# Kernel tuning notes

Measured on AMD Instinct MI355X. Metric: run time of the kernel, lower is better.

The kernel has to match this reference:

```python
import jax, jax.numpy as jnp
import numpy as np

N = 50000      # nodes
E = 800000     # edges
B = 512        # graphs in batch
DRNL = 64      # drnl_dim (feature_dim = 0)
H = 256        # hidden


def setup_inputs() -> dict:
    key = jax.random.key(0)
    ks = jax.random.split(key, 12)
    x = jax.random.normal(ks[0], (N, DRNL), jnp.float32)
    edge_index = jax.random.randint(ks[1], (2, E), 0, N)
    batch_vec = jnp.sort(jax.random.randint(ks[2], (N,), 0, B))
    u_idx = jax.random.randint(ks[3], (B,), 0, N)
    v_idx = jax.random.randint(ks[4], (B,), 0, N)

    def glorot(k, shp):
        scale = jnp.sqrt(2.0 / (shp[0] + shp[1]))
        return (jax.random.normal(k, shp, jnp.float32) * scale).astype(jnp.float32)

    W0 = glorot(ks[5], (DRNL, H)); b0 = jnp.zeros((H,), jnp.float32)
    W1 = glorot(ks[6], (H, H));    b1 = jnp.zeros((H,), jnp.float32)
    W2 = glorot(ks[7], (H, H));    b2 = jnp.zeros((H,), jnp.float32)
    Wm1 = glorot(ks[8], (3 * H, H)); bm1 = jnp.zeros((H,), jnp.float32)
    Wm2 = glorot(ks[9], (H, 1));     bm2 = jnp.zeros((1,), jnp.float32)
    return dict(x=x, edge_index=edge_index, batch_vec=batch_vec,
                u_idx=u_idx, v_idx=v_idx,
                W0=W0, b0=b0, W1=W1, b1=b1, W2=W2, b2=b2,
                Wm1=Wm1, bm1=bm1, Wm2=Wm2, bm2=bm2)


def _gcn_encode(x, src, dst, Ws, bs):
    # Standard GCN: h' = D^-1/2 (A + I) D^-1/2 h W + b, ReLU between layers.
    n = x.shape[0]
    loop = jnp.arange(n)
    src2 = jnp.concatenate([src, loop])  # add self-loops
    dst2 = jnp.concatenate([dst, loop])
    deg = jax.ops.segment_sum(jnp.ones_like(dst2, x.dtype), dst2, num_segments=n)
    dis = jax.lax.rsqrt(jnp.maximum(deg, 1.0))          # D^-1/2
    norm = dis[src2] * dis[dst2]                         # per-edge norm [E+N]

    h = x
    for i, (W, b) in enumerate(zip(Ws, bs)):
        msg = h[src2] * norm[:, None]                    # gather + scale
        agg = jax.ops.segment_sum(msg, dst2, num_segments=n)
        h = agg @ W + b
        if i < len(Ws) - 1:
            h = jax.nn.relu(h)
    return h


def reference(x, edge_index, batch_vec, u_idx, v_idx,
              W0, b0, W1, b1, W2, b2, Wm1, bm1, Wm2, bm2):
    src, dst = edge_index[0], edge_index[1]
    h = _gcn_encode(x, src, dst, (W0, W1, W2), (b0, b1, b2))   # [N, H]

    # global_mean_pool over batch_vec -> [B, H]
    cnt = jax.ops.segment_sum(jnp.ones((h.shape[0],), h.dtype), batch_vec,
                              num_segments=B)
    g = jax.ops.segment_sum(h, batch_vec, num_segments=B) / \
        jnp.maximum(cnt, 1.0)[:, None]

    # concat [g, h[u], h[v]] -> MLP -> [B] logits
    z = jnp.concatenate([g, h[u_idx], h[v_idx]], axis=1)       # [B, 3H]
    z = jax.nn.relu(z @ Wm1 + bm1)
    return (z @ Wm2 + bm2).squeeze(-1)
```

## Files before the change

### kernel.cpp

```cpp
#include <hip/hip_runtime.h>
#include <hip/hip_bf16.h>
#include <stdint.h>

#ifndef DRNL
#define DRNL 64
#define HDIM 256
#endif

#define CHUNK 4096
#define BCAP 3072

typedef __attribute__((ext_vector_type(4))) float f32x4;
typedef __attribute__((ext_vector_type(8))) _Float16 f16x8;

__device__ __forceinline__ void async16(void* lds, const void* g) {
    __builtin_amdgcn_global_load_lds(
        (const __attribute__((address_space(1))) void*)g,
        (__attribute__((address_space(3))) void*)(char*)lds, 16, 0, 0);
}

__device__ __forceinline__ int imin(int a, int b) { return a < b ? a : b; }

__global__ __launch_bounds__(256) void k_misc(
    const int* __restrict__ batch,
    const float* __restrict__ x,
    const float* __restrict__ W0, const float* __restrict__ W1,
    const float* __restrict__ W2,
    int* __restrict__ gstart,
    _Float16* __restrict__ x16,
    _Float16* __restrict__ W0t, _Float16* __restrict__ W1t,
    _Float16* __restrict__ W2t,
    int N, int B) {
    const int gsz = gridDim.x * 256;
    const int gid0 = blockIdx.x * 256 + threadIdx.x;

    for (int i = gid0; i < (DRNL + 2 * HDIM) * 256; i += gsz) {
        int b = i >> 8, c = i & 255;
        const float* W; _Float16* T; int k, K;
        if (b < DRNL)            { W = W0; T = W0t; k = b;              K = DRNL; }
        else if (b < DRNL + 256) { W = W1; T = W1t; k = b - DRNL;       K = HDIM; }
        else                     { W = W2; T = W2t; k = b - DRNL - 256; K = HDIM; }
        T[(size_t)c * K + k] = (_Float16)W[(size_t)k * 256 + c];
    }

    for (int i = gid0; i < N * DRNL; i += gsz) x16[i] = (_Float16)x[i];

    for (int i = gid0; i <= N; i += gsz) {
        if (i == 0) {
            int b0 = batch[0];
            for (int b = 0; b <= b0; ++b) gstart[b] = 0;
        } else if (i == N) {
            int bl = batch[N - 1];
            for (int b = bl + 1; b <= B; ++b) gstart[b] = N;
        } else {
            int bp = batch[i - 1], bc = batch[i];
            if (bc != bp)
                for (int b = bp + 1; b <= bc; ++b) gstart[b] = i;
        }
    }
}

__global__ __launch_bounds__(256) void k_hist(const int* __restrict__ dst,
                                              int* __restrict__ ghist,
                                              int E, int P, int SH, int NBUCK) {
    __shared__ int h[512];
    int tid = threadIdx.x, p = blockIdx.x;
    for (int i = tid; i < NBUCK; i += 256) h[i] = 0;
    __syncthreads();
    int e0 = p * CHUNK, e1 = imin(e0 + CHUNK, E);
    for (int e = e0 + tid; e < e1; e += 256)
        atomicAdd(&h[dst[e] >> SH], 1);
    __syncthreads();
    for (int b = tid; b < NBUCK; b += 256)
        ghist[(size_t)b * P + p] = h[b];
}

__global__ __launch_bounds__(256) void k_gbase(int* __restrict__ ghist,
                                               int* __restrict__ btot, int P) {
    __shared__ int s[256];
    int b = blockIdx.x, tid = threadIdx.x;
    int* row = ghist + (size_t)b * P;
    int carry = 0;
    for (int base = 0; base < P; base += 256) {
        int idx = base + tid;
        int v = (idx < P) ? row[idx] : 0;
        s[tid] = v;
        __syncthreads();
        for (int o = 1; o < 256; o <<= 1) {
            int t = (tid >= o) ? s[tid - o] : 0;
            __syncthreads();
            s[tid] += t;
            __syncthreads();
        }
        if (idx < P) row[idx] = carry + s[tid] - v;
        carry += s[255];
        __syncthreads();
    }
    if (tid == 0) btot[b] = carry;
}

__global__ __launch_bounds__(256) void k_btscan(const int* __restrict__ btot,
                                                int* __restrict__ bbase,
                                                int* __restrict__ rowptr,
                                                int NBUCK, int N, int E) {
    __shared__ int s[256];
    int tid = threadIdx.x;
    int carry = 0;
    for (int base = 0; base < NBUCK; base += 256) {
        int idx = base + tid;
        int v = (idx < NBUCK) ? btot[idx] : 0;
        s[tid] = v;
        __syncthreads();
        for (int o = 1; o < 256; o <<= 1) {
            int t = (tid >= o) ? s[tid - o] : 0;
            __syncthreads();
            s[tid] += t;
            __syncthreads();
        }
        if (idx < NBUCK) bbase[idx] = carry + s[tid] - v;
        carry += s[255];
        __syncthreads();
    }
    if (tid == 0) { bbase[NBUCK] = E; rowptr[N] = E; }
}

__global__ __launch_bounds__(256) void k_scatter(const int* __restrict__ src,
                                                 const int* __restrict__ dst,
                                                 const int* __restrict__ ghist,
                                                 const int* __restrict__ bbase,
                                                 int* __restrict__ tmp,
                                                 int E, int P, int SH, int NBUCK) {
    __shared__ int base[512];
    int p = blockIdx.x, tid = threadIdx.x;
    for (int b = tid; b < NBUCK; b += 256)
        base[b] = bbase[b] + ghist[(size_t)b * P + p];
    __syncthreads();
    int e0 = p * CHUNK, e1 = imin(e0 + CHUNK, E);
    int msk = (1 << SH) - 1;
    for (int e = e0 + tid; e < e1; e += 256) {
        int d = dst[e];
        int r = atomicAdd(&base[d >> SH], 1);
        tmp[r] = (src[e] << SH) | (d & msk);
    }
}

__global__ __launch_bounds__(256) void k_bsort(const int* __restrict__ tmp,
                                               const int* __restrict__ bbase,
                                               int* __restrict__ col,
                                               int* __restrict__ rowptr,
                                               float* __restrict__ dis,
                                               _Float16* __restrict__ x16,
                                               int SH, int N) {
    __shared__ int cnt[512];
    __shared__ int off[512];
    __shared__ int sscan[256];
    __shared__ int eL[BCAP];
    __shared__ unsigned short rnk[BCAP];
    __shared__ int sL[BCAP];
    int b = blockIdx.x, tid = threadIdx.x;
    int nodes = 1 << SH, node0 = b << SH, msk = nodes - 1;
    int lo = bbase[b], hi = bbase[b + 1], m = hi - lo;
    bool fast = (m <= BCAP);

    for (int i = tid; i < nodes; i += 256) cnt[i] = 0;
    __syncthreads();
    if (fast) {
        for (int i = tid; i < m; i += 256) {
            int v = tmp[lo + i];
            eL[i] = v;
            rnk[i] = (unsigned short)atomicAdd(&cnt[v & msk], 1);
        }
    } else {
        for (int i = tid; i < m; i += 256)
            atomicAdd(&cnt[tmp[lo + i] & msk], 1);
    }
    __syncthreads();
    int carry = 0;
    for (int base = 0; base < nodes; base += 256) {
        int idx = base + tid;
        int v = (idx < nodes) ? cnt[idx] : 0;
        sscan[tid] = v;
        __syncthreads();
        for (int o = 1; o < 256; o <<= 1) {
            int t = (tid >= o) ? sscan[tid - o] : 0;
            __syncthreads();
            sscan[tid] += t;
            __syncthreads();
        }
        if (idx < nodes) off[idx] = carry + sscan[tid] - v;
        carry += sscan[255];
        __syncthreads();
    }
    for (int i = tid; i < nodes; i += 256) {
        int node = node0 + i;
        if (node < N) {
            rowptr[node] = lo + off[i];
            dis[node]    = rsqrtf((float)cnt[i] + 1.f);
        }
    }
    int rlim = imin(nodes, N - node0);
    for (int u = tid; u < rlim * 8; u += 256) {
        int r = u >> 3, c = u & 7;
        float d = rsqrtf((float)cnt[r] + 1.f);
        f16x8* xv = (f16x8*)(x16 + (size_t)(node0 + r) * 64);
        f16x8 v = xv[c];
        f16x8 o;
#pragma unroll
        for (int k = 0; k < 8; ++k) o[k] = (_Float16)((float)v[k] * d);
        xv[c] = o;
    }
    __syncthreads();
    if (fast) {
        for (int i = tid; i < m; i += 256) {
            int v = eL[i];
            sL[off[v & msk] + rnk[i]] = v >> SH;
        }
        __syncthreads();
        for (int i = tid; i < m; i += 256) col[lo + i] = sL[i];
    } else {
        for (int i = tid; i < nodes; i += 256) cnt[i] = 0;
        __syncthreads();
        for (int i = tid; i < m; i += 256) {
            int v = tmp[lo + i];
            int d = v & msk;
            int r = atomicAdd(&cnt[d], 1);
            col[lo + off[d] + r] = v >> SH;
        }
    }
}

template <int FBLK>
__global__ __launch_bounds__(256) void k_agg(const _Float16* __restrict__ hs,
                                             const float* __restrict__ dis,
                                             const int* __restrict__ rowptr,
                                             const int* __restrict__ col,
                                             _Float16* __restrict__ A16, int N) {
    int node_wg, f;
    if constexpr (FBLK == 4) {
        int wg = blockIdx.x;
        int xcd = wg & 7;
        f = xcd >> 1;
        int half = xcd & 1;
        int NH = gridDim.x >> 3;
        node_wg = half * NH + (wg >> 3);
    } else {
        node_wg = blockIdx.x;
        f = 0;
    }
    int lane = threadIdx.x & 63;
    int wv = threadIdx.x >> 6;
    int oct = lane >> 3;
    int fl = lane & 7;
    int gw = node_wg * 32 + wv * 8 + oct;
    bool valid = gw < N;
    int gwc = valid ? gw : N - 1;
    const size_t boff = (size_t)f * ((size_t)N * 64);
    const f16x8* hv = (const f16x8*)(hs + boff);
    float acc[8];
#pragma unroll
    for (int k = 0; k < 8; ++k) acc[k] = 0.f;

    int e0 = rowptr[gwc];
    int e1 = valid ? rowptr[gwc + 1] : e0;
    int j = e0;
    while (__any(j < e1)) {
        bool a0 = j < e1, a1 = j + 1 < e1, a2 = j + 2 < e1, a3 = j + 3 < e1;
        int s0 = col[a0 ? j : 0];
        int s1 = col[a1 ? j + 1 : 0];
        int s2 = col[a2 ? j + 2 : 0];
        int s3 = col[a3 ? j + 3 : 0];
        float m0 = a0 ? 1.f : 0.f, m1 = a1 ? 1.f : 0.f;
        float m2 = a2 ? 1.f : 0.f, m3 = a3 ? 1.f : 0.f;
        f16x8 v0 = hv[(size_t)s0 * 8 + fl];
        f16x8 v1 = hv[(size_t)s1 * 8 + fl];
        f16x8 v2 = hv[(size_t)s2 * 8 + fl];
        f16x8 v3 = hv[(size_t)s3 * 8 + fl];
#pragma unroll
        for (int k = 0; k < 8; ++k) acc[k] += m0 * (float)v0[k];
#pragma unroll
        for (int k = 0; k < 8; ++k) acc[k] += m1 * (float)v1[k];
#pragma unroll
        for (int k = 0; k < 8; ++k) acc[k] += m2 * (float)v2[k];
#pragma unroll
        for (int k = 0; k < 8; ++k) acc[k] += m3 * (float)v3[k];
        j += 4;
    }

    float dn = dis[gwc];
    f16x8 hsv = hv[(size_t)gwc * 8 + fl];
    f16x8 o;
#pragma unroll
    for (int k = 0; k < 8; ++k)
        o[k] = (_Float16)((acc[k] + (float)hsv[k]) * dn);
    if (valid)
        __builtin_nontemporal_store(
            o, (f16x8*)(A16 + boff + (size_t)gw * 64 + fl * 8));
}

template <int K, int OUT_RELU, int SCALE>
__global__ __launch_bounds__(256, 2) void k_mgemm(const _Float16* __restrict__ A,
                                                  const _Float16* __restrict__ W,
                                                  const float* __restrict__ bias,
                                                  const float* __restrict__ dis,
                                                  _Float16* __restrict__ outh, int n) {
    __shared__ _Float16 sA[128 * 32];
    __shared__ _Float16 sW[256 * 32];

    const int tid = threadIdx.x;
    const int lane = tid & 63;
    const int w = tid >> 6;
    const int c15 = lane & 15;
    const int q = lane >> 4;
    const int row0 = blockIdx.x * 128;
    const size_t bstride = (size_t)n * 64;

    f32x4 acc[8][4];
#pragma unroll
    for (int i = 0; i < 8; ++i)
#pragma unroll
        for (int j = 0; j < 4; ++j) acc[i][j] = (f32x4)0.f;

    for (int kt = 0; kt < K; kt += 32) {
#pragma unroll
        for (int i = 0; i < 2; ++i) {
            int u = tid + (i << 8);
            int row = u >> 2;
            int qq = (u & 3) ^ ((row >> 1) & 3);
            int r = imin(row0 + row, n - 1);
            size_t goff = (size_t)(kt >> 6) * bstride + (size_t)r * 64 + (kt & 63) + qq * 8;
            async16(sA + u * 8, A + goff);
        }
#pragma unroll
        for (int i = 0; i < 4; ++i) {
            int u = tid + (i << 8);
            int c = u >> 2;
            int qq = (u & 3) ^ ((c >> 1) & 3);
            size_t goff = (size_t)c * K + kt + qq * 8;
            async16(sW + u * 8, W + goff);
        }
        __syncthreads();

        f16x8 wf[4];
#pragma unroll
        for (int ct = 0; ct < 4; ++ct) {
            int c = (w << 6) + (ct << 4) + c15;
            int u = (c << 2) + (q ^ ((c >> 1) & 3));
            wf[ct] = *(const f16x8*)(sW + u * 8);
        }
#pragma unroll
        for (int rt = 0; rt < 8; ++rt) {
            int r = (rt << 4) + c15;
            int u = (r << 2) + (q ^ ((r >> 1) & 3));
            f16x8 a = *(const f16x8*)(sA + u * 8);
#pragma unroll
            for (int ct = 0; ct < 4; ++ct)
                acc[rt][ct] = __builtin_amdgcn_mfma_f32_16x16x32_f16(a, wf[ct], acc[rt][ct], 0, 0, 0);
        }
        __syncthreads();
    }

#pragma unroll
    for (int ct = 0; ct < 4; ++ct) {
        int c = (w << 6) + (ct << 4) + c15;
        float bv = bias[c];
        _Float16* ob = outh + (size_t)(c >> 6) * bstride + (c & 63);
#pragma unroll
        for (int rt = 0; rt < 8; ++rt) {
#pragma unroll
            for (int r = 0; r < 4; ++r) {
                int row = row0 + (rt << 4) + (q << 2) + r;
                if (row < n) {
                    float v = acc[rt][ct][r] + bv;
                    if (OUT_RELU) v = fmaxf(v, 0.f);
                    if (SCALE) v *= dis[row];
                    ob[(size_t)row * 64] = (_Float16)v;
                }
            }
        }
    }
}

__global__ __launch_bounds__(256) void k_head(const _Float16* __restrict__ h,
                                              const int* __restrict__ gstart,
                                              const int* __restrict__ u,
                                              const int* __restrict__ v,
                                              const float* __restrict__ Wm1,
                                              const float* __restrict__ bm1,
                                              const float* __restrict__ Wm2,
                                              const float* __restrict__ bm2,
                                              float* __restrict__ out, int N) {
    int b = blockIdx.x;
    int t = threadIdx.x;
    __shared__ float z[3 * HDIM];
    __shared__ float red[4];
    const _Float16* hb = h + (size_t)(t >> 6) * ((size_t)N * 64) + (t & 63);
    int s = gstart[b], e = gstart[b + 1];
    float pa = 0.f;
    int i = s;
    for (; i + 3 < e; i += 4) {
        float a0 = (float)hb[(size_t)i * 64];
        float a1 = (float)hb[(size_t)(i + 1) * 64];
        float a2 = (float)hb[(size_t)(i + 2) * 64];
        float a3 = (float)hb[(size_t)(i + 3) * 64];
        pa += (a0 + a1) + (a2 + a3);
    }
    for (; i < e; ++i) pa += (float)hb[(size_t)i * 64];
    z[t]            = pa / fmaxf((float)(e - s), 1.f);
    z[HDIM + t]     = (float)hb[(size_t)u[b] * 64];
    z[2 * HDIM + t] = (float)hb[(size_t)v[b] * 64];
    __syncthreads();
    float acc[8];
#pragma unroll
    for (int k = 0; k < 8; ++k) acc[k] = 0.f;
    for (int k = 0; k < 3 * HDIM; k += 8) {
#pragma unroll
        for (int jj = 0; jj < 8; ++jj)
            acc[jj] = fmaf(z[k + jj], Wm1[(size_t)(k + jj) * HDIM + t], acc[jj]);
    }
    float sum = (((acc[0] + acc[1]) + (acc[2] + acc[3])) +
                 ((acc[4] + acc[5]) + (acc[6] + acc[7]))) + bm1[t];
    float hid = fmaxf(sum, 0.f);
    float p = hid * Wm2[t];
    for (int off = 32; off; off >>= 1) p += __shfl_down(p, off);
    if ((t & 63) == 0) red[t >> 6] = p;
    __syncthreads();
    if (t == 0) out[b] = red[0] + red[1] + red[2] + red[3] + bm2[0];
}

extern "C" void kernel_launch(void* const* d_in, const int* in_sizes, int n_in,
                              void* d_out, int out_size, void* d_ws, size_t ws_size,
                              hipStream_t stream) {
    const float* x    = (const float*)d_in[0];
    const int*   ei   = (const int*)d_in[1];
    const int*   batc = (const int*)d_in[2];
    const int*   uidx = (const int*)d_in[3];
    const int*   vidx = (const int*)d_in[4];
    const float* W0   = (const float*)d_in[5];
    const float* b0   = (const float*)d_in[6];
    const float* W1   = (const float*)d_in[7];
    const float* b1   = (const float*)d_in[8];
    const float* W2   = (const float*)d_in[9];
    const float* b2   = (const float*)d_in[10];
    const float* Wm1  = (const float*)d_in[11];
    const float* bm1  = (const float*)d_in[12];
    const float* Wm2  = (const float*)d_in[13];
    const float* bm2  = (const float*)d_in[14];
    float* out = (float*)d_out;

    const int N = in_sizes[0] / DRNL;
    const int E = in_sizes[1] / 2;
    const int B = in_sizes[3];
    const int* src = ei;
    const int* dst = ei + E;

    int SH = 7;
    while (((N + (1 << SH) - 1) >> SH) > 512) ++SH;
    const int NBUCK = (N + (1 << SH) - 1) >> SH;
    const int P = (E + CHUNK - 1) / CHUNK;

    char* w = (char*)d_ws;
    size_t off = 0;
    auto carve = [&](size_t bytes) {
        void* p = w + off;
        off = (off + bytes + 255) & ~(size_t)255;
        return p;
    };
    int*       rowptr = (int*)carve((size_t)(N + 1) * 4);
    int*       colA   = (int*)carve((size_t)E * 4);
    float*     dis    = (float*)carve((size_t)N * 4);
    int*       gstart = (int*)carve((size_t)(B + 1) * 4);
    _Float16*  A16    = (_Float16*)carve((size_t)N * HDIM * 2);
    _Float16*  h16    = (_Float16*)carve((size_t)N * HDIM * 2);
    _Float16*  x16    = (_Float16*)carve((size_t)N * DRNL * 2);
    _Float16*  W0t    = (_Float16*)carve((size_t)DRNL * HDIM * 2);
    _Float16*  W1t    = (_Float16*)carve((size_t)HDIM * HDIM * 2);
    _Float16*  W2t    = (_Float16*)carve((size_t)HDIM * HDIM * 2);
    int*       ghist  = (int*)carve((size_t)NBUCK * P * 4);
    int*       btot   = (int*)carve(512 * 4);
    int*       bbase  = (int*)carve(513 * 4);
    int*       tmpE   = (int*)carve((size_t)E * 4);
    (void)ws_size;

    k_misc<<<1024, 256, 0, stream>>>(batc, x, W0, W1, W2, gstart,
                                     x16, W0t, W1t, W2t, N, B);
    k_hist<<<P, 256, 0, stream>>>(dst, ghist, E, P, SH, NBUCK);
    k_gbase<<<NBUCK, 256, 0, stream>>>(ghist, btot, P);
    k_btscan<<<1, 256, 0, stream>>>(btot, bbase, rowptr, NBUCK, N, E);
    k_scatter<<<P, 256, 0, stream>>>(src, dst, ghist, bbase, tmpE, E, P, SH, NBUCK);
    k_bsort<<<NBUCK, 256, 0, stream>>>(tmpE, bbase, colA, rowptr, dis, x16, SH, N);

    int gemmb = (N + 127) / 128;
    int NB = (N + 31) / 32;
    int NH = (NB + 1) / 2;
    int aggb4 = 8 * NH;

    k_agg<1><<<NB, 256, 0, stream>>>(x16, dis, rowptr, colA, A16, N);
    k_mgemm<DRNL, 1, 1><<<gemmb, 256, 0, stream>>>(A16, W0t, b0, dis, h16, N);
    k_agg<4><<<aggb4, 256, 0, stream>>>(h16, dis, rowptr, colA, A16, N);
    k_mgemm<HDIM, 1, 1><<<gemmb, 256, 0, stream>>>(A16, W1t, b1, dis, h16, N);
    k_agg<4><<<aggb4, 256, 0, stream>>>(h16, dis, rowptr, colA, A16, N);
    k_mgemm<HDIM, 0, 0><<<gemmb, 256, 0, stream>>>(A16, W2t, b2, dis, h16, N);

    k_head<<<B, 256, 0, stream>>>(h16, gstart, uidx, vidx, Wm1, bm1, Wm2, bm2, out, N);
}
```

Baseline: 335.6 us.

## Hold weights in registers per wave and stage GEMM output through LDS

Replaces the LDS-tiled MFMA GEMM with a version where each wave keeps its 64-column slice of W resident in registers for the whole K. A-fragments are loaded directly from global memory, and results are staged in LDS so each row segment is written with coalesced 16-byte stores. The old path wrote scattered single halves. Blocks now cover 64 rows, so the grid doubles. The cost is very high register pressure: K=256 means 32 f16x8 weight fragments per lane, which can lower occupancy or cause spills. The occupancy hint in the launch bounds is also dropped.

```diff
diff --git a/kernel.cpp b/kernel.cpp
--- a/kernel.cpp
+++ b/kernel.cpp
@@ -12,12 +12,6 @@
 
 typedef __attribute__((ext_vector_type(4))) float f32x4;
 typedef __attribute__((ext_vector_type(8))) _Float16 f16x8;
-
-__device__ __forceinline__ void async16(void* lds, const void* g) {
-    __builtin_amdgcn_global_load_lds(
-        (const __attribute__((address_space(1))) void*)g,
-        (__attribute__((address_space(3))) void*)(char*)lds, 16, 0, 0);
-}
 
 __device__ __forceinline__ int imin(int a, int b) { return a < b ? a : b; }
 
@@ -298,85 +292,83 @@
 }
 
 template <int K, int OUT_RELU, int SCALE>
-__global__ __launch_bounds__(256, 2) void k_mgemm(const _Float16* __restrict__ A,
-                                                  const _Float16* __restrict__ W,
-                                                  const float* __restrict__ bias,
-                                                  const float* __restrict__ dis,
-                                                  _Float16* __restrict__ outh, int n) {
-    __shared__ _Float16 sA[128 * 32];
-    __shared__ _Float16 sW[256 * 32];
-
-    const int tid = threadIdx.x;
+__global__ __launch_bounds__(256) void k_wgemm(const _Float16* __restrict__ A,
+                                               const _Float16* __restrict__ W,
+                                               const float* __restrict__ bias,
+                                               const float* __restrict__ dis,
+                                               _Float16* __restrict__ outh, int n) {
+    constexpr int KT = K / 32;
+    __shared__ _Float16 sOut[4 * 16 * 64];
+
+    const int tid  = threadIdx.x;
     const int lane = tid & 63;
-    const int w = tid >> 6;
-    const int c15 = lane & 15;
-    const int q = lane >> 4;
-    const int row0 = blockIdx.x * 128;
+    const int wv   = tid >> 6;
+    const int c15  = lane & 15;
+    const int q    = lane >> 4;
+    const int c0   = wv << 6;
+    const int row0 = blockIdx.x * 64;
     const size_t bstride = (size_t)n * 64;
-
-    f32x4 acc[8][4];
-#pragma unroll
-    for (int i = 0; i < 8; ++i)
-#pragma unroll
-        for (int j = 0; j < 4; ++j) acc[i][j] = (f32x4)0.f;
-
-    for (int kt = 0; kt < K; kt += 32) {
-#pragma unroll
-        for (int i = 0; i < 2; ++i) {
-            int u = tid + (i << 8);
-            int row = u >> 2;
-            int qq = (u & 3) ^ ((row >> 1) & 3);
-            int r = imin(row0 + row, n - 1);
-            size_t goff = (size_t)(kt >> 6) * bstride + (size_t)r * 64 + (kt & 63) + qq * 8;
-            async16(sA + u * 8, A + goff);
-        }
-#pragma unroll
-        for (int i = 0; i < 4; ++i) {
-            int u = tid + (i << 8);
-            int c = u >> 2;
-            int qq = (u & 3) ^ ((c >> 1) & 3);
-            size_t goff = (size_t)c * K + kt + qq * 8;
-            async16(sW + u * 8, W + goff);
-        }
-        __syncthreads();
-
-        f16x8 wf[4];
+    _Float16* sO = sOut + wv * (16 * 64);
+    _Float16* ob = outh + (size_t)wv * bstride;
+
+    f16x8 wf[4][KT];
+#pragma unroll
+    for (int ct = 0; ct < 4; ++ct)
+#pragma unroll
+        for (int kt = 0; kt < KT; ++kt)
+            wf[ct][kt] = *(const f16x8*)(
+                W + (size_t)(c0 + (ct << 4) + c15) * K + (kt << 5) + q * 8);
+
+    float bv[4];
+#pragma unroll
+    for (int ct = 0; ct < 4; ++ct) bv[ct] = bias[c0 + (ct << 4) + c15];
+
+#pragma unroll
+    for (int st = 0; st < 4; ++st) {
+        const int r0 = row0 + (st << 4);
+        const int ra = imin(r0 + c15, n - 1);
+        f16x8 af[KT];
+#pragma unroll
+        for (int kt = 0; kt < KT; ++kt) {
+            const int kk = kt << 5;
+            af[kt] = *(const f16x8*)(A + (size_t)(kk >> 6) * bstride +
+                                     (size_t)ra * 64 + (kk & 63) + q * 8);
+        }
+        f32x4 acc[4];
+#pragma unroll
+        for (int ct = 0; ct < 4; ++ct) acc[ct] = (f32x4)0.f;
+#pragma unroll
+        for (int kt = 0; kt < KT; ++kt)
+#pragma unroll
+            for (int ct = 0; ct < 4; ++ct)
+                acc[ct] = __builtin_amdgcn_mfma_f32_16x16x32_f16(
+                    af[kt], wf[ct][kt], acc[ct], 0, 0, 0);
+
+        float ds[4];
+#pragma unroll
+        for (int r = 0; r < 4; ++r)
+            ds[r] = SCALE ? dis[imin(r0 + (q << 2) + r, n - 1)] : 1.f;
+
 #pragma unroll
         for (int ct = 0; ct < 4; ++ct) {
-            int c = (w << 6) + (ct << 4) + c15;
-            int u = (c << 2) + (q ^ ((c >> 1) & 3));
-            wf[ct] = *(const f16x8*)(sW + u * 8);
-        }
-#pragma unroll
-        for (int rt = 0; rt < 8; ++rt) {
-            int r = (rt << 4) + c15;
-            int u = (r << 2) + (q ^ ((r >> 1) & 3));
-            f16x8 a = *(const f16x8*)(sA + u * 8);
-#pragma unroll
-            for (int ct = 0; ct < 4; ++ct)
-                acc[rt][ct] = __builtin_amdgcn_mfma_f32_16x16x32_f16(a, wf[ct], acc[rt][ct], 0, 0, 0);
-        }
-        __syncthreads();
-    }
-
-#pragma unroll
-    for (int ct = 0; ct < 4; ++ct) {
-        int c = (w << 6) + (ct << 4) + c15;
-        float bv = bias[c];
-        _Float16* ob = outh + (size_t)(c >> 6) * bstride + (c & 63);
-#pragma unroll
-        for (int rt = 0; rt < 8; ++rt) {
 #pragma unroll
             for (int r = 0; r < 4; ++r) {
-                int row = row0 + (rt << 4) + (q << 2) + r;
-                if (row < n) {
-                    float v = acc[rt][ct][r] + bv;
-                    if (OUT_RELU) v = fmaxf(v, 0.f);
-                    if (SCALE) v *= dis[row];
-                    ob[(size_t)row * 64] = (_Float16)v;
-                }
+                float v = acc[ct][r] + bv[ct];
+                if (OUT_RELU) v = fmaxf(v, 0.f);
+                v *= ds[r];
+                sO[((q << 2) + r) * 64 + (ct << 4) + c15] = (_Float16)v;
             }
         }
+        __syncthreads();
+#pragma unroll
+        for (int ps = 0; ps < 2; ++ps) {
+            int u = (ps << 6) + lane;
+            int rr = u >> 3, ch = u & 7;
+            f16x8 vv = *(const f16x8*)(sO + rr * 64 + ch * 8);
+            if (r0 + rr < n)
+                *(f16x8*)(ob + (size_t)(r0 + rr) * 64 + ch * 8) = vv;
+        }
+        __syncthreads();
     }
 }
 
@@ -489,17 +481,17 @@
     k_scatter<<<P, 256, 0, stream>>>(src, dst, ghist, bbase, tmpE, E, P, SH, NBUCK);
     k_bsort<<<NBUCK, 256, 0, stream>>>(tmpE, bbase, colA, rowptr, dis, x16, SH, N);
 
-    int gemmb = (N + 127) / 128;
+    int gemmb = (N + 63) / 64;
     int NB = (N + 31) / 32;
     int NH = (NB + 1) / 2;
     int aggb4 = 8 * NH;
 
     k_agg<1><<<NB, 256, 0, stream>>>(x16, dis, rowptr, colA, A16, N);
-    k_mgemm<DRNL, 1, 1><<<gemmb, 256, 0, stream>>>(A16, W0t, b0, dis, h16, N);
+    k_wgemm<DRNL, 1, 1><<<gemmb, 256, 0, stream>>>(A16, W0t, b0, dis, h16, N);
     k_agg<4><<<aggb4, 256, 0, stream>>>(h16, dis, rowptr, colA, A16, N);
-    k_mgemm<HDIM, 1, 1><<<gemmb, 256, 0, stream>>>(A16, W1t, b1, dis, h16, N);
+    k_wgemm<HDIM, 1, 1><<<gemmb, 256, 0, stream>>>(A16, W1t, b1, dis, h16, N);
     k_agg<4><<<aggb4, 256, 0, stream>>>(h16, dis, rowptr, colA, A16, N);
-    k_mgemm<HDIM, 0, 0><<<gemmb, 256, 0, stream>>>(A16, W2t, b2, dis, h16, N);
+    k_wgemm<HDIM, 0, 0><<<gemmb, 256, 0, stream>>>(A16, W2t, b2, dis, h16, N);
 
     k_head<<<B, 256, 0, stream>>>(h16, gstart, uidx, vidx, Wm1, bm1, Wm2, bm2, out, N);
 }
```

New measurement: 341.8 us. Within noise of the previous version (+1.8%).
